# Kernel tuning notes

Measured on AMD Instinct MI355X. Metric: run time of the kernel, lower is better.

Reference implementation:

```python
import jax, jax.numpy as jnp
import numpy as np

B, S, D = 2, 1024, 1024
H, KVH, HD = 16, 4, 64  # query heads, kv heads, head_dim
EPS = 1e-5
SCALE = float(np.sqrt(HD))  # note: scale uses original head_dim, not concat dim


def rmsnorm(x, g):
    return x * jax.lax.rsqrt(jnp.mean(x * x, axis=-1, keepdims=True) + EPS) * g


def rope(x, cos, sin):
    # x: [B,S,h,HD]; cos/sin: [S, HD//2]; pairs are consecutive (view_as_complex layout)
    xr = x.reshape(*x.shape[:-1], HD // 2, 2)
    x0, x1 = xr[..., 0], xr[..., 1]
    c = cos[None, :, None, :]
    s = sin[None, :, None, :]
    o0 = x0 * c - x1 * s
    o1 = x0 * s + x1 * c
    return jnp.stack([o0, o1], axis=-1).reshape(x.shape)


def context_build(x, W, gq, gk):
    comb = x @ W.T  # [B,S, H*HD + 2*KVH*HD]
    q, k, v = jnp.split(comb, [H * HD, H * HD + KVH * HD], axis=-1)
    q = rmsnorm(q, gq).reshape(B, S, H, HD)
    k = rmsnorm(k, gk).reshape(B, S, KVH, HD)
    v = v.reshape(B, S, KVH, HD)
    return q, k, v


def setup_inputs() -> dict:
    key = jax.random.key(0)
    ks = jax.random.split(key, 12)
    total = H * HD + 2 * KVH * HD  # 1536
    pos = jnp.arange(S, dtype=jnp.float32)
    theta = 10000.0 ** (-jnp.arange(0, HD, 2, dtype=jnp.float32) / HD)  # [HD//2]
    ang = pos[:, None] * theta[None, :]  # [S, HD//2]
    sc = 0.02
    return {
        "local_c": jax.random.normal(ks[0], (B, S, D), jnp.float32),
        "global_c": jax.random.normal(ks[1], (B, S, D), jnp.float32),
        "freqs_cos": jnp.cos(ang),
        "freqs_sin": jnp.sin(ang),
        "W_lc": jax.random.normal(ks[2], (total, D), jnp.float32) * sc,
        "W_gc": jax.random.normal(ks[3], (total, D), jnp.float32) * sc,
        "g_q_lc": jnp.ones((H * HD,), jnp.float32),
        "g_k_lc": jnp.ones((KVH * HD,), jnp.float32),
        "g_q_gc": jnp.ones((H * HD,), jnp.float32),
        "g_k_gc": jnp.ones((KVH * HD,), jnp.float32),
        "W_local": jax.random.normal(ks[4], (H * HD, 2 * H * HD), jnp.float32) * sc,
        "b_local": jnp.zeros((H * HD,), jnp.float32),
        "g_lc_out": jnp.ones((H * HD,), jnp.float32),
        "W_global": jax.random.normal(ks[5], (H * HD, 2 * H * HD), jnp.float32) * sc,
        "b_global": jnp.zeros((H * HD,), jnp.float32),
        "g_gc_out": jnp.ones((H * HD,), jnp.float32),
    }


def reference(local_c, global_c, freqs_cos, freqs_sin, W_lc, W_gc,
              g_q_lc, g_k_lc, g_q_gc, g_k_gc,
              W_local, b_local, g_lc_out, W_global, b_global, g_gc_out):
    q_lc, k_lc, v_lc = context_build(local_c, W_lc, g_q_lc, g_k_lc)
    q_gc, k_gc, v_gc = context_build(global_c, W_gc, g_q_gc, g_k_gc)

    q_lc = rope(q_lc, freqs_cos, freqs_sin)
    k_lc = rope(k_lc, freqs_cos, freqs_sin)
    q_gc = rope(q_gc, freqs_cos, freqs_sin)
    k_gc = rope(k_gc, freqs_cos, freqs_sin)

    # concat local+global along head_dim -> per-head dim 2*HD
    q = jnp.concatenate([q_lc, q_gc], axis=-1)  # [B,S,H,2HD]
    k = jnp.concatenate([k_lc, k_gc], axis=-1)  # [B,S,KVH,2HD]
    v = jnp.concatenate([v_lc, v_gc], axis=-1)

    n_rep = H // KVH
    k = jnp.repeat(k, n_rep, axis=2)  # [B,S,H,2HD] (GQA repeat_kv)
    v = jnp.repeat(v, n_rep, axis=2)

    scores = jnp.einsum("bqhd,bkhd->bhqk", q, k) / SCALE  # [B,H,S,S]
    attn = jax.nn.softmax(scores, axis=-1)
    out = jnp.einsum("bhqk,bkhd->bqhd", attn, v).reshape(B, S, H * 2 * HD)

    x_lc = rmsnorm(out @ W_local.T + b_local, g_lc_out)
    x_gc = rmsnorm(out @ W_global.T + b_global, g_gc_out)
    return (x_lc, x_gc)
```

## Files before the change

kernel.cpp:

```cpp
#include <hip/hip_runtime.h>

typedef __attribute__((ext_vector_type(8))) __bf16 bf16x8;
typedef __attribute__((ext_vector_type(4))) __bf16 bf16x4;
typedef __attribute__((ext_vector_type(4))) float f32x4;

__device__ __forceinline__ bf16x8 cvt8(const float* __restrict__ p)
{
    const float4 a = *(const float4*)p;
    const float4 b = *(const float4*)(p + 4);
    bf16x8 r;
    r[0] = (__bf16)a.x; r[1] = (__bf16)a.y; r[2] = (__bf16)a.z; r[3] = (__bf16)a.w;
    r[4] = (__bf16)b.x; r[5] = (__bf16)b.y; r[6] = (__bf16)b.z; r[7] = (__bf16)b.w;
    return r;
}

__device__ __forceinline__ void gld16(const __bf16* g, __bf16* l)
{
    __builtin_amdgcn_global_load_lds(
        (const __attribute__((address_space(1))) void*)g,
        (__attribute__((address_space(3))) void*)l, 16, 0, 0);
}

struct CvtArgs {
    const float* s[6];
    __bf16* d[6];
    int n[6];
};

__global__ __launch_bounds__(256) void cvt_bf16(CvtArgs a)
{
    const int t = blockIdx.y;
    const int i0 = (blockIdx.x * 256 + threadIdx.x) * 8;
    if (i0 < a.n[t])
        *(bf16x8*)(a.d[t] + i0) = cvt8(a.s[t] + i0);
}

template <typename CT>
__device__ __forceinline__ void gemm_core(const __bf16* __restrict__ Ap, int lda,
                                          const __bf16* __restrict__ Bp, int ldb,
                                          CT* __restrict__ Cp, int ldc, int K)
{
    __shared__ __bf16 As[2][128 * 32];
    __shared__ __bf16 Bs[2][128 * 32];
    const int tid  = threadIdx.x;
    const int w    = tid >> 6;
    const int lane = tid & 63;
    const int ln   = lane & 15;
    const int quad = lane >> 4;
    const int wm   = w & 1;
    const int wn   = w >> 1;

    const int srow = 32 * w + (lane >> 2);
    const int scol = (lane & 3) * 8;

    f32x4 acc[4][4];
    const f32x4 zero = {0.f, 0.f, 0.f, 0.f};
#pragma unroll
    for (int i = 0; i < 4; i++)
#pragma unroll
        for (int j = 0; j < 4; j++) acc[i][j] = zero;

    auto stage = [&](int buf, int k0) {
        gld16(Ap + (size_t)srow * lda        + k0 + scol, As[buf] + (2 * w)     * 512 + lane * 8);
        gld16(Ap + (size_t)(srow + 16) * lda + k0 + scol, As[buf] + (2 * w + 1) * 512 + lane * 8);
        gld16(Bp + (size_t)srow * ldb        + k0 + scol, Bs[buf] + (2 * w)     * 512 + lane * 8);
        gld16(Bp + (size_t)(srow + 16) * ldb + k0 + scol, Bs[buf] + (2 * w + 1) * 512 + lane * 8);
    };

    stage(0, 0);
    int buf = 0;
    for (int k0 = 0; k0 < K; k0 += 32, buf ^= 1) {
        __syncthreads();
        if (k0 + 32 < K) stage(buf ^ 1, k0 + 32);

        bf16x8 af[4], bw[4];
#pragma unroll
        for (int i = 0; i < 4; i++)
            af[i] = *(const bf16x8*)(As[buf] + (wm * 64 + i * 16 + ln) * 32 + quad * 8);
#pragma unroll
        for (int j = 0; j < 4; j++)
            bw[j] = *(const bf16x8*)(Bs[buf] + (wn * 64 + j * 16 + ln) * 32 + quad * 8);
#pragma unroll
        for (int i = 0; i < 4; i++)
#pragma unroll
            for (int j = 0; j < 4; j++)
                acc[i][j] = __builtin_amdgcn_mfma_f32_16x16x32_bf16(
                    af[i], bw[j], acc[i][j], 0, 0, 0);
    }

#pragma unroll
    for (int i = 0; i < 4; i++)
#pragma unroll
        for (int j = 0; j < 4; j++)
#pragma unroll
            for (int r = 0; r < 4; r++) {
                const int ml = wm * 64 + i * 16 + quad * 4 + r;
                const int nl = wn * 64 + j * 16 + ln;
                Cp[(size_t)ml * ldc + nl] = (CT)acc[i][j][r];
            }
}

__global__ __launch_bounds__(256) void gemm_qkv(const __bf16* __restrict__ Xbf,
                                                const __bf16* __restrict__ Wqkv,
                                                __bf16* __restrict__ comb)
{
    const int z = blockIdx.z;
    const __bf16* A = Xbf  + (size_t)z * 2048 * 1024 + (size_t)blockIdx.y * 128 * 1024;
    const __bf16* B = Wqkv + (size_t)z * 1536 * 1024 + (size_t)blockIdx.x * 128 * 1024;
    __bf16* C = comb + (size_t)z * 2048 * 1536 +
                (size_t)blockIdx.y * 128 * 1536 + (size_t)blockIdx.x * 128;
    gemm_core<__bf16>(A, 1024, B, 1024, C, 1536, 1024);
}

__global__ __launch_bounds__(256) void gemm_out(const __bf16* __restrict__ AO,
                                                const __bf16* __restrict__ Wout,
                                                __bf16* __restrict__ Y0,
                                                __bf16* __restrict__ Y1)
{
    const int kh = blockIdx.z;
    const __bf16* A = AO   + (size_t)blockIdx.y * 128 * 2048 + kh * 1024;
    const __bf16* B = Wout + (size_t)blockIdx.x * 128 * 2048 + kh * 1024;
    __bf16* Y = kh ? Y1 : Y0;
    __bf16* C = Y + (size_t)blockIdx.y * 128 * 2048 + (size_t)blockIdx.x * 128;
    gemm_core<__bf16>(A, 2048, B, 2048, C, 2048, 1024);
}

__global__ __launch_bounds__(256) void pack_qkv(
    const __bf16* __restrict__ comb,
    const float* __restrict__ fcos, const float* __restrict__ fsin,
    const float* __restrict__ g_q_lc, const float* __restrict__ g_k_lc,
    const float* __restrict__ g_q_gc, const float* __restrict__ g_k_gc,
    __bf16* __restrict__ Qb, __bf16* __restrict__ Kb, __bf16* __restrict__ Vb)
{
    const int m = blockIdx.x, ctx = blockIdx.y;
    const int b = m >> 10, s = m & 1023;
    const int tid = threadIdx.x;
    const __bf16* cr = comb + ((size_t)ctx * 2048 + m) * 1536;
    const float* gq = ctx ? g_q_gc : g_q_lc;
    const float* gk = ctx ? g_k_gc : g_k_lc;

    const bf16x4 qv = *(const bf16x4*)(cr + tid * 4);
    float sq = (float)qv[0] * (float)qv[0] + (float)qv[1] * (float)qv[1] +
               (float)qv[2] * (float)qv[2] + (float)qv[3] * (float)qv[3];
    const float kvv = (float)cr[1024 + tid];
    float sk = kvv * kvv;
#pragma unroll
    for (int off = 32; off > 0; off >>= 1) {
        sq += __shfl_down(sq, off);
        sk += __shfl_down(sk, off);
    }
    __shared__ float redq[4], redk[4];
    if ((tid & 63) == 0) { redq[tid >> 6] = sq; redk[tid >> 6] = sk; }
    __syncthreads();
    sq = redq[0] + redq[1] + redq[2] + redq[3];
    sk = redk[0] + redk[1] + redk[2] + redk[3];
    const float rq = rsqrtf(sq * (1.f / 1024.f) + 1e-5f);
    const float rk = rsqrtf(sk * (1.f / 256.f) + 1e-5f);

#pragma unroll
    for (int pp = 0; pp < 2; pp++) {
        const int p = tid + pp * 256;
        const int h = p >> 5, pi = p & 31;
        const float x0 = (float)cr[2 * p]     * rq * gq[2 * p];
        const float x1 = (float)cr[2 * p + 1] * rq * gq[2 * p + 1];
        const float c  = fcos[s * 32 + pi];
        const float sn = fsin[s * 32 + pi];
        const float o0 = (x0 * c - x1 * sn) * 0.125f;
        const float o1 = (x0 * sn + x1 * c) * 0.125f;
        const size_t qo = ((size_t)m * 16 + h) * 128 + ctx * 64 + 2 * pi;
        Qb[qo]     = (__bf16)o0;
        Qb[qo + 1] = (__bf16)o1;
    }
    if (tid < 128) {
        const int p = tid;
        const int kvh = p >> 5, pi = p & 31;
        const float x0 = (float)cr[1024 + 2 * p]     * rk * gk[2 * p];
        const float x1 = (float)cr[1024 + 2 * p + 1] * rk * gk[2 * p + 1];
        const float c  = fcos[s * 32 + pi];
        const float sn = fsin[s * 32 + pi];
        const float o0 = x0 * c - x1 * sn;
        const float o1 = x0 * sn + x1 * c;
        const size_t ko = ((size_t)(b * 4 + kvh) * 1024 + s) * 128 + ctx * 64 + 2 * pi;
        Kb[ko]     = (__bf16)o0;
        Kb[ko + 1] = (__bf16)o1;
    }
    {
        const int kvh = tid >> 6, d = tid & 63;
        Vb[((size_t)(b * 4 + kvh) * 1024 + s) * 128 + ctx * 64 + d] = cr[1280 + tid];
    }
}

__global__ __launch_bounds__(256) void v_transpose(const __bf16* __restrict__ Vb,
                                                   __bf16* __restrict__ Vtb)
{
    __shared__ __bf16 lds[64 * 64];
    const int st  = blockIdx.x;
    const int dt  = blockIdx.y;
    const int bkv = blockIdx.z;
    const int tid = threadIdx.x;
    const __bf16* src = Vb  + ((size_t)bkv * 1024 + st * 64) * 128 + dt * 64;
    __bf16*       dst = Vtb + ((size_t)bkv * 128 + dt * 64) * 1024 + st * 64;

#pragma unroll
    for (int i = 0; i < 2; i++) {
        const int c = tid + i * 256;
        const int s_in = c >> 3, ch = c & 7;
        const bf16x8 v = *(const bf16x8*)(src + (size_t)s_in * 128 + ch * 8);
        *(bf16x8*)&lds[s_in * 64 + (((ch + (s_in >> 3)) & 7) * 8)] = v;
    }
    __syncthreads();
#pragma unroll
    for (int i = 0; i < 2; i++) {
        const int c = tid + i * 256;
        const int dd = c >> 3, s0 = (c & 7) * 8;
        bf16x8 o;
#pragma unroll
        for (int jj = 0; jj < 8; jj++) {
            const int s = s0 + jj;
            o[jj] = lds[s * 64 + ((((dd >> 3) + (s >> 3)) & 7) * 8) + (dd & 7)];
        }
        *(bf16x8*)(dst + (size_t)dd * 1024 + s0) = o;
    }
}

__global__ __launch_bounds__(512, 4) void attn(const __bf16* __restrict__ Qb,
                                               const __bf16* __restrict__ Kb,
                                               const __bf16* __restrict__ Vtb,
                                               __bf16* __restrict__ AO)
{
    __shared__ __align__(16) __bf16 Ks[2][64][132];
    __shared__ __align__(16) __bf16 Vts[2][128][72];
    __shared__ __align__(16) __bf16 Ps[8][16][36];
    __shared__ float Lsum[2][4][16];

    const int tid  = threadIdx.x;
    const int w    = tid >> 6;
    const int wq   = w >> 1;
    const int wk   = w & 1;
    const int lane = tid & 63;
    const int ln   = lane & 15;
    const int quad = lane >> 4;
    const int qt = blockIdx.x, h = blockIdx.y, b = blockIdx.z;
    const int kv = h >> 2;

    const __bf16* Kbase = Kb  + (size_t)(b * 4 + kv) * 1024 * 128;
    const __bf16* Vbase = Vtb + (size_t)(b * 4 + kv) * 128 * 1024;

    bf16x8 qf[4];
    {
        const int qrow = qt * 64 + wq * 16 + ln;
        const __bf16* qptr = Qb + ((size_t)(b * 1024 + qrow) * 16 + h) * 128;
#pragma unroll
        for (int kc = 0; kc < 4; kc++)
            qf[kc] = *(const bf16x8*)(qptr + kc * 32 + quad * 8);
    }

    f32x4 oacc[8];
    const f32x4 zero = {0.f, 0.f, 0.f, 0.f};
#pragma unroll
    for (int j = 0; j < 8; j++) oacc[j] = zero;
    float lpart[4] = {0.f, 0.f, 0.f, 0.f};

    bf16x8 kreg[2], vreg[2];
    auto load_tiles = [&](int kt) {
        const int ks0 = kt * 64;
#pragma unroll
        for (int i = 0; i < 2; i++) {
            const int c = tid + i * 512;
            kreg[i] = *(const bf16x8*)(Kbase + (size_t)(ks0 + (c >> 4)) * 128 + (c & 15) * 8);
            vreg[i] = *(const bf16x8*)(Vbase + (size_t)(c >> 3) * 1024 + ks0 + (c & 7) * 8);
        }
    };
    auto write_tiles = [&](int buf) {
#pragma unroll
        for (int i = 0; i < 2; i++) {
            const int c = tid + i * 512;
            *(bf16x8*)&Ks[buf][c >> 4][(c & 15) * 8] = kreg[i];
            *(bf16x8*)&Vts[buf][c >> 3][(c & 7) * 8] = vreg[i];
        }
    };

    load_tiles(0);
    write_tiles(0);

    for (int kt = 0; kt < 16; kt++) {
        const int buf = kt & 1;
        if (kt + 1 < 16) load_tiles(kt + 1);

        asm volatile("s_waitcnt lgkmcnt(0)\n\ts_barrier" ::: "memory");

        f32x4 sacc[2];
        __builtin_amdgcn_s_setprio(1);
#pragma unroll
        for (int j = 0; j < 2; j++) {
            f32x4 a = zero;
#pragma unroll
            for (int kc = 0; kc < 4; kc++) {
                const bf16x8 kf =
                    *(const bf16x8*)&Ks[buf][wk * 32 + j * 16 + ln][kc * 32 + quad * 8];
                a = __builtin_amdgcn_mfma_f32_16x16x32_bf16(qf[kc], kf, a, 0, 0, 0);
            }
            sacc[j] = a;
        }
        __builtin_amdgcn_s_setprio(0);

#pragma unroll
        for (int j = 0; j < 2; j++)
#pragma unroll
            for (int r = 0; r < 4; r++) {
                const float p = __expf(sacc[j][r] - 20.f);
                lpart[r] += p;
                Ps[w][quad * 4 + r][j * 16 + ln] = (__bf16)p;
            }

        const bf16x8 pf = *(const bf16x8*)&Ps[w][ln][quad * 8];
        __builtin_amdgcn_s_setprio(1);
#pragma unroll
        for (int j2 = 0; j2 < 8; j2++) {
            const bf16x8 vf =
                *(const bf16x8*)&Vts[buf][j2 * 16 + ln][wk * 32 + quad * 8];
            oacc[j2] = __builtin_amdgcn_mfma_f32_16x16x32_bf16(pf, vf, oacc[j2], 0, 0, 0);
        }
        __builtin_amdgcn_s_setprio(0);

        if (kt + 1 < 16) write_tiles(buf ^ 1);
    }

    float lrow[4];
#pragma unroll
    for (int r = 0; r < 4; r++) {
        float rs = lpart[r];
#pragma unroll
        for (int off = 1; off < 16; off <<= 1)
            rs += __shfl_xor(rs, off);
        lrow[r] = rs;
    }
    if (ln == 0) {
#pragma unroll
        for (int r = 0; r < 4; r++)
            Lsum[wk][wq][quad * 4 + r] = lrow[r];
    }
    __syncthreads();

    float* scr = (float*)&Vts[0][0][0];
    if (wk == 1) {
#pragma unroll
        for (int j2 = 0; j2 < 8; j2++)
#pragma unroll
            for (int r = 0; r < 4; r++)
                scr[(wq * 16 + quad * 4 + r) * 132 + j2 * 16 + ln] = oacc[j2][r];
    }
    __syncthreads();
    if (wk == 0) {
        float inv[4];
#pragma unroll
        for (int r = 0; r < 4; r++)
            inv[r] = 1.f / (Lsum[0][wq][quad * 4 + r] + Lsum[1][wq][quad * 4 + r]);
#pragma unroll
        for (int j2 = 0; j2 < 8; j2++)
#pragma unroll
            for (int r = 0; r < 4; r++) {
                const float v = oacc[j2][r] +
                    scr[(wq * 16 + quad * 4 + r) * 132 + j2 * 16 + ln];
                const size_t row = (size_t)(b * 1024 + qt * 64 + wq * 16 + quad * 4 + r);
                AO[row * 2048 + h * 128 + j2 * 16 + ln] = (__bf16)(v * inv[r]);
            }
    }
}

__global__ __launch_bounds__(256) void rmsnorm_out(const __bf16* __restrict__ Y0,
                                                   const __bf16* __restrict__ Y1,
                                                   const float* __restrict__ b_l,
                                                   const float* __restrict__ b_g,
                                                   const float* __restrict__ g_l,
                                                   const float* __restrict__ g_g,
                                                   float* __restrict__ out)
{
    const int m = blockIdx.x, which = blockIdx.y;
    const int tid = threadIdx.x;
    const size_t off = (size_t)m * 2048 + which * 1024 + tid * 4;
    const float* bias = which ? b_g : b_l;
    const float* g    = which ? g_g : g_l;

    const bf16x4 y0 = *(const bf16x4*)(Y0 + off);
    const bf16x4 y1 = *(const bf16x4*)(Y1 + off);
    const float4 bv = *(const float4*)(bias + tid * 4);
    float x[4];
    x[0] = (float)y0[0] + (float)y1[0] + bv.x;
    x[1] = (float)y0[1] + (float)y1[1] + bv.y;
    x[2] = (float)y0[2] + (float)y1[2] + bv.z;
    x[3] = (float)y0[3] + (float)y1[3] + bv.w;
    float ss = x[0] * x[0] + x[1] * x[1] + x[2] * x[2] + x[3] * x[3];
#pragma unroll
    for (int off2 = 32; off2 > 0; off2 >>= 1) ss += __shfl_down(ss, off2);
    __shared__ float red[4];
    if ((tid & 63) == 0) red[tid >> 6] = ss;
    __syncthreads();
    ss = red[0] + red[1] + red[2] + red[3];
    const float r = rsqrtf(ss * (1.f / 1024.f) + 1e-5f);

    const float4 gv = *(const float4*)(g + tid * 4);
    float4 o;
    o.x = x[0] * r * gv.x;
    o.y = x[1] * r * gv.y;
    o.z = x[2] * r * gv.z;
    o.w = x[3] * r * gv.w;
    *(float4*)(out + (size_t)which * 2097152 + (size_t)m * 1024 + tid * 4) = o;
}

extern "C" void kernel_launch(void* const* d_in, const int* in_sizes, int n_in,
                              void* d_out, int out_size, void* d_ws, size_t ws_size,
                              hipStream_t stream)
{
    (void)in_sizes; (void)n_in; (void)out_size; (void)ws_size;
    const float* local_c  = (const float*)d_in[0];
    const float* global_c = (const float*)d_in[1];
    const float* fcos     = (const float*)d_in[2];
    const float* fsin     = (const float*)d_in[3];
    const float* W_lc     = (const float*)d_in[4];
    const float* W_gc     = (const float*)d_in[5];
    const float* g_q_lc   = (const float*)d_in[6];
    const float* g_k_lc   = (const float*)d_in[7];
    const float* g_q_gc   = (const float*)d_in[8];
    const float* g_k_gc   = (const float*)d_in[9];
    const float* W_local  = (const float*)d_in[10];
    const float* b_local  = (const float*)d_in[11];
    const float* g_lc_out = (const float*)d_in[12];
    const float* W_global = (const float*)d_in[13];
    const float* b_global = (const float*)d_in[14];
    const float* g_gc_out = (const float*)d_in[15];

    char* ws = (char*)d_ws;
    __bf16* Wout = (__bf16*)(ws + 0);
    __bf16* Xbf  = (__bf16*)(ws + 8388608);
    __bf16* Wqkv = (__bf16*)(ws + 16777216);
    __bf16* comb = (__bf16*)(ws + 23068672);
    __bf16* Qb   = (__bf16*)(ws + 35651584);
    __bf16* Kb   = (__bf16*)(ws + 44040192);
    __bf16* Vtb  = (__bf16*)(ws + 46137344);
    __bf16* AO   = (__bf16*)(ws + 48234496);
    __bf16* Y0   = (__bf16*)(ws + 56623104);
    __bf16* Y1   = (__bf16*)(ws + 65011712);
    __bf16* Vb   = (__bf16*)(ws + 56623104);

    CvtArgs ca;
    ca.s[0] = local_c;  ca.d[0] = Xbf;            ca.n[0] = 2097152;
    ca.s[1] = global_c; ca.d[1] = Xbf + 2097152;  ca.n[1] = 2097152;
    ca.s[2] = W_lc;     ca.d[2] = Wqkv;           ca.n[2] = 1572864;
    ca.s[3] = W_gc;     ca.d[3] = Wqkv + 1572864; ca.n[3] = 1572864;
    ca.s[4] = W_local;  ca.d[4] = Wout;           ca.n[4] = 2097152;
    ca.s[5] = W_global; ca.d[5] = Wout + 2097152; ca.n[5] = 2097152;

    cvt_bf16<<<dim3(1024, 6), 256, 0, stream>>>(ca);
    gemm_qkv<<<dim3(12, 16, 2), 256, 0, stream>>>(Xbf, Wqkv, comb);
    pack_qkv<<<dim3(2048, 2), 256, 0, stream>>>(comb, fcos, fsin,
                                                g_q_lc, g_k_lc, g_q_gc, g_k_gc,
                                                Qb, Kb, Vb);
    v_transpose<<<dim3(16, 2, 8), 256, 0, stream>>>(Vb, Vtb);
    attn<<<dim3(16, 16, 2), 512, 0, stream>>>(Qb, Kb, Vtb, AO);
    gemm_out<<<dim3(16, 16, 2), 256, 0, stream>>>(AO, Wout, Y0, Y1);
    rmsnorm_out<<<dim3(2048, 2), 256, 0, stream>>>(Y0, Y1, b_local, b_global,
                                                   g_lc_out, g_gc_out,
                                                   (float*)d_out);
}
```

Measured before the change: 212.5 us.

## Use direct global-to-LDS loads with XOR swizzle in attention and remap GEMM block order

The attention kernel now stages K and V tiles with global_load_lds 16-byte async copies straight into unpadded, XOR-swizzled LDS buffers. This replaces the register round-trip and the separate LDS write step, and the staging of the next tile is issued right after the barrier. The QKV GEMM, output GEMM and attention kernels also remap their flat block index so that consecutively launched blocks are spread across the same XCD, aiming for better L2 reuse. The risks are the wait semantics of the async LDS loads against __syncthreads, and a larger LDS footprint that may reduce occupancy.

```diff
diff --git a/kernel.cpp b/kernel.cpp
--- a/kernel.cpp
+++ b/kernel.cpp
@@ -104,11 +104,13 @@
                                                 const __bf16* __restrict__ Wqkv,
                                                 __bf16* __restrict__ comb)
 {
-    const int z = blockIdx.z;
-    const __bf16* A = Xbf  + (size_t)z * 2048 * 1024 + (size_t)blockIdx.y * 128 * 1024;
-    const __bf16* B = Wqkv + (size_t)z * 1536 * 1024 + (size_t)blockIdx.x * 128 * 1024;
+    const int flat = (blockIdx.z * 16 + blockIdx.y) * 12 + blockIdx.x;
+    const int l  = (flat % 8) * 48 + flat / 8;
+    const int bx = l % 12, by = (l / 12) % 16, z = l / 192;
+    const __bf16* A = Xbf  + (size_t)z * 2048 * 1024 + (size_t)by * 128 * 1024;
+    const __bf16* B = Wqkv + (size_t)z * 1536 * 1024 + (size_t)bx * 128 * 1024;
     __bf16* C = comb + (size_t)z * 2048 * 1536 +
-                (size_t)blockIdx.y * 128 * 1536 + (size_t)blockIdx.x * 128;
+                (size_t)by * 128 * 1536 + (size_t)bx * 128;
     gemm_core<__bf16>(A, 1024, B, 1024, C, 1536, 1024);
 }
 
@@ -117,11 +119,13 @@
                                                 __bf16* __restrict__ Y0,
                                                 __bf16* __restrict__ Y1)
 {
-    const int kh = blockIdx.z;
-    const __bf16* A = AO   + (size_t)blockIdx.y * 128 * 2048 + kh * 1024;
-    const __bf16* B = Wout + (size_t)blockIdx.x * 128 * 2048 + kh * 1024;
+    const int flat = (blockIdx.z * 16 + blockIdx.y) * 16 + blockIdx.x;
+    const int l  = (flat & 7) * 64 + (flat >> 3);
+    const int bx = l & 15, by = (l >> 4) & 15, kh = l >> 8;
+    const __bf16* A = AO   + (size_t)by * 128 * 2048 + kh * 1024;
+    const __bf16* B = Wout + (size_t)bx * 128 * 2048 + kh * 1024;
     __bf16* Y = kh ? Y1 : Y0;
-    __bf16* C = Y + (size_t)blockIdx.y * 128 * 2048 + (size_t)blockIdx.x * 128;
+    __bf16* C = Y + (size_t)by * 128 * 2048 + (size_t)bx * 128;
     gemm_core<__bf16>(A, 2048, B, 2048, C, 2048, 1024);
 }
 
@@ -228,10 +232,11 @@
                                                const __bf16* __restrict__ Vtb,
                                                __bf16* __restrict__ AO)
 {
-    __shared__ __align__(16) __bf16 Ks[2][64][132];
-    __shared__ __align__(16) __bf16 Vts[2][128][72];
-    __shared__ __align__(16) __bf16 Ps[8][16][36];
-    __shared__ float Lsum[2][4][16];
+    __shared__ __align__(16) char smem[75264];
+    __bf16* Ks   = (__bf16*)smem;
+    __bf16* Vts  = (__bf16*)(smem + 32768);
+    __bf16* Ps   = (__bf16*)(smem + 65536);
+    float*  Lsum = (float*)(smem + 74752);
 
     const int tid  = threadIdx.x;
     const int w    = tid >> 6;
@@ -240,7 +245,11 @@
     const int lane = tid & 63;
     const int ln   = lane & 15;
     const int quad = lane >> 4;
-    const int qt = blockIdx.x, h = blockIdx.y, b = blockIdx.z;
+    const int lx   = ln & 7;
+
+    const int flat = (blockIdx.z * 16 + blockIdx.y) * 16 + blockIdx.x;
+    const int lid  = (flat & 7) * 64 + (flat >> 3);
+    const int qt = lid & 15, h = (lid >> 4) & 15, b = lid >> 8;
     const int kv = h >> 2;
 
     const __bf16* Kbase = Kb  + (size_t)(b * 4 + kv) * 1024 * 128;
@@ -261,43 +270,37 @@
     for (int j = 0; j < 8; j++) oacc[j] = zero;
     float lpart[4] = {0.f, 0.f, 0.f, 0.f};
 
-    bf16x8 kreg[2], vreg[2];
-    auto load_tiles = [&](int kt) {
+    auto stage = [&](int buf, int kt) {
         const int ks0 = kt * 64;
 #pragma unroll
         for (int i = 0; i < 2; i++) {
-            const int c = tid + i * 512;
-            kreg[i] = *(const bf16x8*)(Kbase + (size_t)(ks0 + (c >> 4)) * 128 + (c & 15) * 8);
-            vreg[i] = *(const bf16x8*)(Vbase + (size_t)(c >> 3) * 1024 + ks0 + (c & 7) * 8);
+            const int l = tid + i * 512;
+            const int kr = l >> 4, kx = l & 15;
+            gld16(Kbase + (size_t)(ks0 + kr) * 128 + ((kx ^ (kr & 7)) * 8),
+                  Ks + buf * 8192 + l * 8);
+            const int vr = l >> 3, vx = l & 7;
+            gld16(Vbase + (size_t)vr * 1024 + ks0 + ((vx ^ (vr & 7)) * 8),
+                  Vts + buf * 8192 + l * 8);
         }
     };
-    auto write_tiles = [&](int buf) {
-#pragma unroll
-        for (int i = 0; i < 2; i++) {
-            const int c = tid + i * 512;
-            *(bf16x8*)&Ks[buf][c >> 4][(c & 15) * 8] = kreg[i];
-            *(bf16x8*)&Vts[buf][c >> 3][(c & 7) * 8] = vreg[i];
-        }
-    };
-
-    load_tiles(0);
-    write_tiles(0);
+
+    stage(0, 0);
 
     for (int kt = 0; kt < 16; kt++) {
         const int buf = kt & 1;
-        if (kt + 1 < 16) load_tiles(kt + 1);
-
-        asm volatile("s_waitcnt lgkmcnt(0)\n\ts_barrier" ::: "memory");
+        __syncthreads();
+        if (kt + 1 < 16) stage(buf ^ 1, kt + 1);
 
         f32x4 sacc[2];
         __builtin_amdgcn_s_setprio(1);
 #pragma unroll
         for (int j = 0; j < 2; j++) {
+            const __bf16* krow = Ks + buf * 8192 + (wk * 32 + j * 16 + ln) * 128;
             f32x4 a = zero;
 #pragma unroll
             for (int kc = 0; kc < 4; kc++) {
                 const bf16x8 kf =
-                    *(const bf16x8*)&Ks[buf][wk * 32 + j * 16 + ln][kc * 32 + quad * 8];
+                    *(const bf16x8*)(krow + (((kc * 4 + quad) ^ lx) * 8));
                 a = __builtin_amdgcn_mfma_f32_16x16x32_bf16(qf[kc], kf, a, 0, 0, 0);
             }
             sacc[j] = a;
@@ -310,20 +313,19 @@
             for (int r = 0; r < 4; r++) {
                 const float p = __expf(sacc[j][r] - 20.f);
                 lpart[r] += p;
-                Ps[w][quad * 4 + r][j * 16 + ln] = (__bf16)p;
+                Ps[(w * 16 + quad * 4 + r) * 36 + j * 16 + ln] = (__bf16)p;
             }
 
-        const bf16x8 pf = *(const bf16x8*)&Ps[w][ln][quad * 8];
+        const bf16x8 pf = *(const bf16x8*)(Ps + (w * 16 + ln) * 36 + quad * 8);
+        const int vco = ((wk * 4 + quad) ^ lx) * 8;
         __builtin_amdgcn_s_setprio(1);
 #pragma unroll
         for (int j2 = 0; j2 < 8; j2++) {
             const bf16x8 vf =
-                *(const bf16x8*)&Vts[buf][j2 * 16 + ln][wk * 32 + quad * 8];
+                *(const bf16x8*)(Vts + buf * 8192 + (j2 * 16 + ln) * 64 + vco);
             oacc[j2] = __builtin_amdgcn_mfma_f32_16x16x32_bf16(pf, vf, oacc[j2], 0, 0, 0);
         }
         __builtin_amdgcn_s_setprio(0);
-
-        if (kt + 1 < 16) write_tiles(buf ^ 1);
     }
 
     float lrow[4];
@@ -338,11 +340,11 @@
     if (ln == 0) {
 #pragma unroll
         for (int r = 0; r < 4; r++)
-            Lsum[wk][wq][quad * 4 + r] = lrow[r];
+            Lsum[(wk * 4 + wq) * 16 + quad * 4 + r] = lrow[r];
     }
     __syncthreads();
 
-    float* scr = (float*)&Vts[0][0][0];
+    float* scr = (float*)smem;
     if (wk == 1) {
 #pragma unroll
         for (int j2 = 0; j2 < 8; j2++)
@@ -355,7 +357,8 @@
         float inv[4];
 #pragma unroll
         for (int r = 0; r < 4; r++)
-            inv[r] = 1.f / (Lsum[0][wq][quad * 4 + r] + Lsum[1][wq][quad * 4 + r]);
+            inv[r] = 1.f / (Lsum[(0 + wq) * 16 + quad * 4 + r] +
+                            Lsum[(4 + wq) * 16 + quad * 4 + r]);
 #pragma unroll
         for (int j2 = 0; j2 < 8; j2++)
 #pragma unroll
```

After: 207.9 us. 2.1% less time.
